# Kernel optimization log

Hardware: AMD Instinct MI355X
Metric: run time of the kernel (lower is better)

The kernel has to match this reference:

```python
import jax, jax.numpy as jnp
import numpy as np

N = 100000  # num_nodes


def setup_inputs() -> dict:
    key = jax.random.key(0)
    k1, k2, k3, k4 = jax.random.split(key, 4)
    nodes = jax.random.randint(k1, (10000,), 0, N)
    edge_index = jax.random.randint(k2, (2, 1600000), 0, N)
    emb_weight = jax.random.normal(k3, (N, 512), dtype=jnp.float32)
    W = jax.random.normal(k4, (512, 128), dtype=jnp.float32) * 0.05
    return {"nodes": nodes, "edge_index": edge_index, "emb_weight": emb_weight, "W": W}


def reference(nodes, edge_index, emb_weight, W):
    # GCNConv (PyG semantics, bias=False): add self-loops, symmetric deg
    # normalization, linear transform, scatter-add aggregation into targets.
    num_nodes = emb_weight.shape[0]
    loops = jnp.arange(num_nodes, dtype=edge_index.dtype)
    row = jnp.concatenate([edge_index[0], loops])  # sources (x_j)
    col = jnp.concatenate([edge_index[1], loops])  # targets (aggregation)

    ones = jnp.ones(row.shape[0], dtype=emb_weight.dtype)
    deg = jax.ops.segment_sum(ones, col, num_segments=num_nodes)
    dinv = jnp.where(deg > 0, jax.lax.rsqrt(deg), 0.0)
    norm = dinv[row] * dinv[col]  # [E+N]

    h = emb_weight @ W  # [N, C] dense transform (main GEMM)
    msg = h[row] * norm[:, None]  # gather + scale, [E+N, C]
    out = jax.ops.segment_sum(msg, col, num_segments=num_nodes)  # scatter-add
    return out[nodes]
```

## Files before the change

kernel.cpp:

```cpp
#include <hip/hip_runtime.h>
#include <hip/hip_bf16.h>


constexpr int KDIM = 512;
constexpr int CDIM = 128;
constexpr int CAPB = 64;
constexpr int CAPO = 16;
constexpr int NCPY = 8;

typedef __attribute__((ext_vector_type(8))) short short8;
typedef __attribute__((ext_vector_type(4))) float f32x4;

static __device__ __forceinline__ unsigned short f2bf(float f) {
    __hip_bfloat16 b = __float2bfloat16(f);
    return *reinterpret_cast<unsigned short*>(&b);
}
static __device__ __forceinline__ float bf2f(unsigned short b) {
    return __uint_as_float(((unsigned)b) << 16);
}

__global__ void k_init(int* __restrict__ deg8, int* __restrict__ tmap,
                       int* __restrict__ cur, int* __restrict__ ocnt,
                       int* __restrict__ ucount,
                       const float* __restrict__ W, unsigned short* __restrict__ wt,
                       int N, int n) {
    int i = blockIdx.x * blockDim.x + threadIdx.x;
    if (i < NCPY * N) deg8[i] = 0;
    if (i < N) tmap[i] = -1;
    if (i < n) { cur[i] = 0; ocnt[i] = 0; }
    if (i == 0) *ucount = 0;
    if (i < 65536) {
        int j  = i & 7;
        int l  = (i >> 3) & 63;
        int st = i >> 9;
        int t  = st & 7, s = st >> 3;
        int k  = s * 32 + (l >> 4) * 8 + j;
        int c  = t * 16 + (l & 15);
        wt[i] = f2bf(W[(size_t)k * CDIM + c]);
    }
}

__global__ void k_targets(const int* __restrict__ nodes, int n,
                          int* __restrict__ tmap, int* __restrict__ tlist,
                          int* __restrict__ ucount) {
    int i = blockIdx.x * blockDim.x + threadIdx.x;
    if (i >= n) return;
    int v = nodes[i];
    if (atomicCAS(&tmap[v], -1, -2) == -1) {
        int slot = atomicAdd(ucount, 1);
        tlist[slot] = v;
        tmap[v] = slot;
    }
}

__global__ void k_dsum(const int* __restrict__ deg8, float* __restrict__ dinv, int N) {
    int i = blockIdx.x * blockDim.x + threadIdx.x;
    if (i >= N) return;
    int s = 0;
    #pragma unroll
    for (int x = 0; x < NCPY; ++x) s += deg8[(size_t)x * N + i];
    dinv[i] = rsqrtf((float)(s + 1));
}

__global__ __launch_bounds__(512, 2)
void k_main(const float* __restrict__ emb, const unsigned short* __restrict__ wt,
            unsigned short* __restrict__ h, int N,
            const int* __restrict__ erow, const int* __restrict__ ecol, int E,
            int* __restrict__ deg8, const int* __restrict__ tmap,
            int* __restrict__ cur, int* __restrict__ ebuf,
            const int* __restrict__ nodes, int n,
            int* __restrict__ ocnt, int* __restrict__ olist,
            int GB, int DB) {
    int bid = (int)blockIdx.x;
    if (bid >= GB + DB) {
        int i = (bid - GB - DB) * 512 + threadIdx.x;
        if (i >= n) return;
        int slot = tmap[nodes[i]];
        int p = atomicAdd(&ocnt[slot], 1);
        if (p < CAPO) olist[slot * CAPO + p] = i;
        return;
    }
    if (bid >= GB) {
        int* dp = deg8 + (size_t)(bid & (NCPY - 1)) * N;
        int t = (bid - GB) * 512 + threadIdx.x;
        int base = t * 4;
        if (base >= E) return;
        if (base + 4 <= E) {
            int4 c = *reinterpret_cast<const int4*>(ecol + base);
            atomicAdd(&dp[c.x], 1);
            atomicAdd(&dp[c.y], 1);
            atomicAdd(&dp[c.z], 1);
            atomicAdd(&dp[c.w], 1);
            int s0 = tmap[c.x], s1 = tmap[c.y], s2 = tmap[c.z], s3 = tmap[c.w];
            if ((s0 >= 0) | (s1 >= 0) | (s2 >= 0) | (s3 >= 0)) {
                int4 r = *reinterpret_cast<const int4*>(erow + base);
                if (s0 >= 0) { int p = atomicAdd(&cur[s0], 1); if (p < CAPB) ebuf[s0 * CAPB + p] = r.x; }
                if (s1 >= 0) { int p = atomicAdd(&cur[s1], 1); if (p < CAPB) ebuf[s1 * CAPB + p] = r.y; }
                if (s2 >= 0) { int p = atomicAdd(&cur[s2], 1); if (p < CAPB) ebuf[s2 * CAPB + p] = r.z; }
                if (s3 >= 0) { int p = atomicAdd(&cur[s3], 1); if (p < CAPB) ebuf[s3 * CAPB + p] = r.w; }
            }
        } else {
            for (int i = base; i < E; ++i) {
                int c = ecol[i];
                atomicAdd(&dp[c], 1);
                int s = tmap[c];
                if (s >= 0) { int p = atomicAdd(&cur[s], 1); if (p < CAPB) ebuf[s * CAPB + p] = erow[i]; }
            }
        }
        return;
    }
    extern __shared__ char smem[];
    float*          sA = (float*)smem;
    unsigned short* sB = (unsigned short*)(smem + 3 * 16384);
    int tid  = threadIdx.x;
    int lane = tid & 63;
    int wid  = tid >> 6;
    int row0 = bid * 128;

    auto stage = [&](int buf, int kc) {
        #pragma unroll
        for (int p = 0; p < 2; ++p) {
            int i = p * 512 + tid;
            int row = i >> 3, chunk = i & 7;
            int swz = chunk ^ (row & 7);
            int rg = row0 + row; if (rg >= N) rg = N - 1;
            const float* g = emb + (size_t)rg * KDIM + kc * 32 + swz * 4;
            float* l = sA + buf * 4096 + i * 4;
            __builtin_amdgcn_global_load_lds(
                (const __attribute__((address_space(1))) void*)g,
                (__attribute__((address_space(3))) void*)l, 16, 0, 0);
        }
        {
            const unsigned short* g = wt + (size_t)kc * 4096 + tid * 8;
            unsigned short* l = sB + buf * 4096 + tid * 8;
            __builtin_amdgcn_global_load_lds(
                (const __attribute__((address_space(1))) void*)g,
                (__attribute__((address_space(3))) void*)l, 16, 0, 0);
        }
    };

    f32x4 acc[8];
    #pragma unroll
    for (int t = 0; t < 8; ++t) acc[t] = (f32x4){0.f, 0.f, 0.f, 0.f};

    int arow = wid * 16 + (lane & 15);
    int kq   = lane >> 4;

    auto compute = [&](int buf) {
        const float*          Ab = sA + buf * 4096;
        const unsigned short* Bb = sB + buf * 4096;
        int c0 = kq * 2;
        int s0 = c0 ^ (arow & 7);
        int s1 = (c0 + 1) ^ (arow & 7);
        float4 v0 = *reinterpret_cast<const float4*>(Ab + arow * 32 + s0 * 4);
        float4 v1 = *reinterpret_cast<const float4*>(Ab + arow * 32 + s1 * 4);
        short8 af;
        af[0] = (short)f2bf(v0.x); af[1] = (short)f2bf(v0.y);
        af[2] = (short)f2bf(v0.z); af[3] = (short)f2bf(v0.w);
        af[4] = (short)f2bf(v1.x); af[5] = (short)f2bf(v1.y);
        af[6] = (short)f2bf(v1.z); af[7] = (short)f2bf(v1.w);
        #pragma unroll
        for (int tt = 0; tt < 8; ++tt) {
            short8 bf = *reinterpret_cast<const short8*>(Bb + ((size_t)(tt * 64 + lane)) * 8);
            acc[tt] = __builtin_amdgcn_mfma_f32_16x16x32_bf16(af, bf, acc[tt], 0, 0, 0);
        }
    };

    stage(0, 0); stage(1, 1); stage(2, 2);

    for (int kc = 0; kc < 14; ++kc) {
        if (kc > 0) stage((kc + 2) % 3, kc + 2);
        asm volatile("s_waitcnt vmcnt(6)" ::: "memory");
        __builtin_amdgcn_s_barrier();
        asm volatile("" ::: "memory");
        compute(kc % 3);
        asm volatile("" ::: "memory");
        __builtin_amdgcn_s_barrier();
    }
    asm volatile("s_waitcnt vmcnt(3)" ::: "memory");
    __builtin_amdgcn_s_barrier();
    asm volatile("" ::: "memory");
    compute(2);
    asm volatile("" ::: "memory");
    __builtin_amdgcn_s_barrier();
    asm volatile("s_waitcnt vmcnt(0)" ::: "memory");
    __builtin_amdgcn_s_barrier();
    asm volatile("" ::: "memory");
    compute(0);

    __syncthreads();
    unsigned short* sC = (unsigned short*)smem;
    int rl0 = wid * 16 + (lane >> 4) * 4;
    int cl0 = lane & 15;
    #pragma unroll
    for (int tt = 0; tt < 8; ++tt)
        #pragma unroll
        for (int j = 0; j < 4; ++j)
            sC[(rl0 + j) * 128 + cl0 + tt * 16] = f2bf(acc[tt][j]);
    __syncthreads();
    #pragma unroll
    for (int c = 0; c < 4; ++c) {
        int i = c * 512 + tid;
        int row = i >> 4, off = i & 15;
        int r = row0 + row;
        if (r < N)
            *reinterpret_cast<short8*>(h + (size_t)r * CDIM + off * 8) =
                *reinterpret_cast<const short8*>(sC + row * 128 + off * 8);
    }
}

__global__ __launch_bounds__(256)
void k_agg(const unsigned short* __restrict__ h, const float* __restrict__ dinv,
           const int* __restrict__ tlist, const int* __restrict__ cur,
           const int* __restrict__ ebuf, const int* __restrict__ ucount,
           const int* __restrict__ ocnt, const int* __restrict__ olist,
           float* __restrict__ out) {
    int u = *ucount;
    int slot = blockIdx.x * 4 + (threadIdx.x >> 6);
    if (slot >= u) return;
    int lane = threadIdx.x & 63;
    int e = min(cur[slot], CAPB);
    int myi = 0; float myw = 0.f;
    if (lane < e) {
        myi = ebuf[(size_t)slot * CAPB + lane];
        myw = dinv[myi];
    }
    int q  = lane >> 4;
    int cl = lane & 15;
    float acc[8];
    #pragma unroll
    for (int x = 0; x < 8; ++x) acc[x] = 0.f;
    int trips = (e + 3) >> 2;
    for (int t = 0; t < trips; ++t) {
        int j = t * 4 + q;
        int   src = __shfl(myi, j, 64);
        float w   = __shfl(myw, j, 64);
        short8 v = *reinterpret_cast<const short8*>(h + (size_t)src * CDIM + cl * 8);
        #pragma unroll
        for (int x = 0; x < 8; ++x)
            acc[x] += w * bf2f((unsigned short)v[x]);
    }
    #pragma unroll
    for (int x = 0; x < 8; ++x) {
        acc[x] += __shfl_xor(acc[x], 16, 64);
        acc[x] += __shfl_xor(acc[x], 32, 64);
    }
    int t = tlist[slot];
    float dt = dinv[t];
    short8 v = *reinterpret_cast<const short8*>(h + (size_t)t * CDIM + cl * 8);
    float4 r0, r1;
    r0.x = dt * (acc[0] + dt * bf2f((unsigned short)v[0]));
    r0.y = dt * (acc[1] + dt * bf2f((unsigned short)v[1]));
    r0.z = dt * (acc[2] + dt * bf2f((unsigned short)v[2]));
    r0.w = dt * (acc[3] + dt * bf2f((unsigned short)v[3]));
    r1.x = dt * (acc[4] + dt * bf2f((unsigned short)v[4]));
    r1.y = dt * (acc[5] + dt * bf2f((unsigned short)v[5]));
    r1.z = dt * (acc[6] + dt * bf2f((unsigned short)v[6]));
    r1.w = dt * (acc[7] + dt * bf2f((unsigned short)v[7]));
    if (q == 0) {
        int cnt = min(ocnt[slot], CAPO);
        for (int qq = 0; qq < cnt; ++qq) {
            int i = olist[slot * CAPO + qq];
            float* op = out + (size_t)i * CDIM + cl * 8;
            *reinterpret_cast<float4*>(op)     = r0;
            *reinterpret_cast<float4*>(op + 4) = r1;
        }
    }
}

extern "C" void kernel_launch(void* const* d_in, const int* in_sizes, int n_in,
                              void* d_out, int out_size, void* d_ws, size_t ws_size,
                              hipStream_t stream) {
    const int*   nodes = (const int*)d_in[0];
    const int*   eidx  = (const int*)d_in[1];
    const float* emb   = (const float*)d_in[2];
    const float* W     = (const float*)d_in[3];
    float*       out   = (float*)d_out;

    int n = in_sizes[0];
    int E = in_sizes[1] / 2;
    int N = in_sizes[2] / KDIM;
    const int* erow = eidx;
    const int* ecol = eidx + E;

    char* ws = (char*)d_ws;
    size_t o = 0;
    auto carve = [&](size_t bytes) {
        char* p = ws + o;
        o = (o + bytes + 255) & ~(size_t)255;
        return p;
    };
    int*   deg8  = (int*)carve((size_t)NCPY * N * 4);
    float* dinv  = (float*)carve((size_t)N * 4);
    int*   tmap  = (int*)carve((size_t)N * 4);
    int*   tlist = (int*)carve((size_t)n * 4);
    int*   cur   = (int*)carve((size_t)n * 4);
    int*   ocnt  = (int*)carve((size_t)n * 4);
    int*   olist = (int*)carve((size_t)n * CAPO * 4);
    int*   ucount= (int*)carve(4);
    int*   ebuf  = (int*)carve((size_t)n * CAPB * 4);
    unsigned short* wt = (unsigned short*)carve((size_t)16 * 8 * 64 * 8 * 2);
    unsigned short* h  = (unsigned short*)carve((size_t)N * CDIM * 2);
    (void)ws_size; (void)n_in; (void)out_size;

    hipFuncSetAttribute(reinterpret_cast<const void*>(k_main),
                        hipFuncAttributeMaxDynamicSharedMemorySize, 73728);

    int GB = (N + 127) / 128;
    int DB = (E + 2047) / 2048;
    int OB = (n + 511) / 512;
    k_init   <<<(NCPY * N + 255) / 256, 256, 0, stream>>>(deg8, tmap, cur, ocnt, ucount,
                                                          W, wt, N, n);
    k_targets<<<(n + 255) / 256, 256, 0, stream>>>(nodes, n, tmap, tlist, ucount);
    k_main   <<<GB + DB + OB, 512, 73728, stream>>>(emb, wt, h, N,
                                                    erow, ecol, E, deg8, tmap, cur, ebuf,
                                                    nodes, n, ocnt, olist, GB, DB);
    k_dsum   <<<(N + 255) / 256, 256, 0, stream>>>(deg8, dinv, N);
    k_agg    <<<(n + 3) / 4, 256, 0, stream>>>(h, dinv, tlist, cur, ebuf, ucount,
                                               ocnt, olist, out);
}
```

Before: 128.7 us.

## Fold edge-binning and output-list work into GEMM blocks as a prologue

Removes the separate edge-processing and output-list blocks from the main launch. Each GEMM block now first handles a 2048-edge chunk (degree atomics and target binning) plus a small slice of the output-node list, then runs its GEMM tile. The grid shrinks to the GEMM block count, which avoids scheduling many short-lived blocks next to the LDS-heavy GEMM blocks. The cost is that each GEMM block waits on scattered atomics before its GEMM starts. Edge coverage now relies on GB*2048 >= E, which holds for these sizes but not in general.

```diff
diff --git a/kernel.cpp b/kernel.cpp
--- a/kernel.cpp
+++ b/kernel.cpp
@@ -70,49 +70,51 @@
             int* __restrict__ cur, int* __restrict__ ebuf,
             const int* __restrict__ nodes, int n,
             int* __restrict__ ocnt, int* __restrict__ olist,
-            int GB, int DB) {
+            int GB, int OM) {
+    extern __shared__ char smem[];
     int bid = (int)blockIdx.x;
-    if (bid >= GB + DB) {
-        int i = (bid - GB - DB) * 512 + threadIdx.x;
-        if (i >= n) return;
-        int slot = tmap[nodes[i]];
-        int p = atomicAdd(&ocnt[slot], 1);
-        if (p < CAPO) olist[slot * CAPO + p] = i;
-        return;
-    }
-    if (bid >= GB) {
+    int tid = threadIdx.x;
+
+    {
+        int idx = bid * OM + tid;
+        if (tid < OM && idx < n) {
+            int slot = tmap[nodes[idx]];
+            int p = atomicAdd(&ocnt[slot], 1);
+            if (p < CAPO) olist[slot * CAPO + p] = idx;
+        }
+    }
+    {
         int* dp = deg8 + (size_t)(bid & (NCPY - 1)) * N;
-        int t = (bid - GB) * 512 + threadIdx.x;
-        int base = t * 4;
-        if (base >= E) return;
-        if (base + 4 <= E) {
-            int4 c = *reinterpret_cast<const int4*>(ecol + base);
-            atomicAdd(&dp[c.x], 1);
-            atomicAdd(&dp[c.y], 1);
-            atomicAdd(&dp[c.z], 1);
-            atomicAdd(&dp[c.w], 1);
-            int s0 = tmap[c.x], s1 = tmap[c.y], s2 = tmap[c.z], s3 = tmap[c.w];
-            if ((s0 >= 0) | (s1 >= 0) | (s2 >= 0) | (s3 >= 0)) {
-                int4 r = *reinterpret_cast<const int4*>(erow + base);
-                if (s0 >= 0) { int p = atomicAdd(&cur[s0], 1); if (p < CAPB) ebuf[s0 * CAPB + p] = r.x; }
-                if (s1 >= 0) { int p = atomicAdd(&cur[s1], 1); if (p < CAPB) ebuf[s1 * CAPB + p] = r.y; }
-                if (s2 >= 0) { int p = atomicAdd(&cur[s2], 1); if (p < CAPB) ebuf[s2 * CAPB + p] = r.z; }
-                if (s3 >= 0) { int p = atomicAdd(&cur[s3], 1); if (p < CAPB) ebuf[s3 * CAPB + p] = r.w; }
+        int base = bid * 2048 + tid * 4;
+        if (base < E) {
+            if (base + 4 <= E) {
+                int4 c = *reinterpret_cast<const int4*>(ecol + base);
+                atomicAdd(&dp[c.x], 1);
+                atomicAdd(&dp[c.y], 1);
+                atomicAdd(&dp[c.z], 1);
+                atomicAdd(&dp[c.w], 1);
+                int s0 = tmap[c.x], s1 = tmap[c.y], s2 = tmap[c.z], s3 = tmap[c.w];
+                if ((s0 >= 0) | (s1 >= 0) | (s2 >= 0) | (s3 >= 0)) {
+                    int4 r = *reinterpret_cast<const int4*>(erow + base);
+                    if (s0 >= 0) { int p = atomicAdd(&cur[s0], 1); if (p < CAPB) ebuf[s0 * CAPB + p] = r.x; }
+                    if (s1 >= 0) { int p = atomicAdd(&cur[s1], 1); if (p < CAPB) ebuf[s1 * CAPB + p] = r.y; }
+                    if (s2 >= 0) { int p = atomicAdd(&cur[s2], 1); if (p < CAPB) ebuf[s2 * CAPB + p] = r.z; }
+                    if (s3 >= 0) { int p = atomicAdd(&cur[s3], 1); if (p < CAPB) ebuf[s3 * CAPB + p] = r.w; }
+                }
+            } else {
+                for (int i = base; i < E; ++i) {
+                    int c = ecol[i];
+                    atomicAdd(&dp[c], 1);
+                    int s = tmap[c];
+                    if (s >= 0) { int p = atomicAdd(&cur[s], 1); if (p < CAPB) ebuf[s * CAPB + p] = erow[i]; }
+                }
             }
-        } else {
-            for (int i = base; i < E; ++i) {
-                int c = ecol[i];
-                atomicAdd(&dp[c], 1);
-                int s = tmap[c];
-                if (s >= 0) { int p = atomicAdd(&cur[s], 1); if (p < CAPB) ebuf[s * CAPB + p] = erow[i]; }
-            }
-        }
-        return;
-    }
-    extern __shared__ char smem[];
+        }
+    }
+    asm volatile("s_waitcnt vmcnt(0)" ::: "memory");
+
     float*          sA = (float*)smem;
     unsigned short* sB = (unsigned short*)(smem + 3 * 16384);
-    int tid  = threadIdx.x;
     int lane = tid & 63;
     int wid  = tid >> 6;
     int row0 = bid * 128;
@@ -307,14 +309,13 @@
                         hipFuncAttributeMaxDynamicSharedMemorySize, 73728);
 
     int GB = (N + 127) / 128;
-    int DB = (E + 2047) / 2048;
-    int OB = (n + 511) / 512;
+    int OM = (n + GB - 1) / GB;
     k_init   <<<(NCPY * N + 255) / 256, 256, 0, stream>>>(deg8, tmap, cur, ocnt, ucount,
                                                           W, wt, N, n);
     k_targets<<<(n + 255) / 256, 256, 0, stream>>>(nodes, n, tmap, tlist, ucount);
-    k_main   <<<GB + DB + OB, 512, 73728, stream>>>(emb, wt, h, N,
-                                                    erow, ecol, E, deg8, tmap, cur, ebuf,
-                                                    nodes, n, ocnt, olist, GB, DB);
+    k_main   <<<GB, 512, 73728, stream>>>(emb, wt, h, N,
+                                          erow, ecol, E, deg8, tmap, cur, ebuf,
+                                          nodes, n, ocnt, olist, GB, OM);
     k_dsum   <<<(N + 255) / 256, 256, 0, stream>>>(deg8, dinv, N);
     k_agg    <<<(n + 3) / 4, 256, 0, stream>>>(h, dinv, tlist, cur, ebuf, ucount,
                                                ocnt, olist, out);
```

New measurement: 139.6 us. 8.4% more time.
